# Kernel tuning notes

Hardware: AMD Instinct MI355X
Metric: run time of the kernel (lower is better)

Reference implementation:

```python
import jax, jax.numpy as jnp
import numpy as np

B, S, U = 64, 64, 16
EMB = 10
D = U - 2 + 2 * EMB      # encoder d_model = 34
DD = 3                   # decoder d_model
FF = 4                   # dim_feedforward
NL = 4                   # num layers (enc and dec)
ENH = 2                  # encoder heads
WV, SV = 10000, 400      # word / syllable vocab sizes


def _ln(x, w, b, eps=1e-5):
    mu = jnp.mean(x, -1, keepdims=True)
    var = jnp.mean((x - mu) ** 2, -1, keepdims=True)
    return (x - mu) / jnp.sqrt(var + eps) * w + b


def _mha(xq, xkv, qkv_w, qkv_b, out_w, out_b, nhead, mask=None):
    d = xq.shape[-1]
    wq, wk, wv = jnp.split(qkv_w, 3, axis=0)
    bq, bk, bv = jnp.split(qkv_b, 3, axis=0)
    q = xq @ wq.T + bq
    k = xkv @ wk.T + bk
    v = xkv @ wv.T + bv
    b_, sq, sk = q.shape[0], q.shape[1], k.shape[1]
    dh = d // nhead
    q = q.reshape(b_, sq, nhead, dh)
    k = k.reshape(b_, sk, nhead, dh)
    v = v.reshape(b_, sk, nhead, dh)
    scores = jnp.einsum('bqhd,bkhd->bhqk', q, k) * (1.0 / np.sqrt(dh))
    if mask is not None:
        scores = scores + mask
    attn = jax.nn.softmax(scores, axis=-1)
    out = jnp.einsum('bhqk,bkhd->bqhd', attn, v).reshape(b_, sq, d)
    return out @ out_w.T + out_b


def _pos_encoding(batch, d_model):
    # Faithful to the original quirk: pe has shape [max_len, 1, d] and is added
    # to a batch-first [B,S,D] tensor as x + pe[:B]  ->  row b of pe is added
    # to ALL sequence positions of batch element b.
    pos = jnp.arange(batch, dtype=jnp.float32)[:, None]
    div = jnp.exp(jnp.arange(0, d_model, 2, dtype=jnp.float32) * (-np.log(10000.0) / d_model))
    ang = pos * div  # [B, D/2]
    pe = jnp.stack([jnp.sin(ang), jnp.cos(ang)], axis=-1).reshape(batch, d_model)
    return pe[:, None, :]  # [B,1,D]


def setup_inputs() -> dict:
    key = jax.random.key(0)
    ks = iter(jax.random.split(key, 64))

    def n(shape, s=0.1):
        return jax.random.normal(next(ks), shape, dtype=jnp.float32) * s

    base = jax.random.uniform(next(ks), (B, S, U), dtype=jnp.float32)
    widx = jax.random.randint(next(ks), (B, S), 0, WV).astype(jnp.float32)
    sidx = jax.random.randint(next(ks), (B, S), 0, SV).astype(jnp.float32)
    src = base.at[:, :, U - 2].set(widx).at[:, :, U - 1].set(sidx)
    return {
        'src': src,
        'word_emb': jax.random.uniform(next(ks), (WV, EMB), jnp.float32, -0.1, 0.1),
        'syll_emb': jax.random.uniform(next(ks), (SV, EMB), jnp.float32, -0.1, 0.1),
        'enc_qkv_w': n((NL, 3 * D, D)), 'enc_qkv_b': jnp.zeros((NL, 3 * D)),
        'enc_out_w': n((NL, D, D)), 'enc_out_b': jnp.zeros((NL, D)),
        'enc_ln1_w': jnp.ones((NL, D)), 'enc_ln1_b': jnp.zeros((NL, D)),
        'enc_lin1_w': n((NL, FF, D)), 'enc_lin1_b': jnp.zeros((NL, FF)),
        'enc_lin2_w': n((NL, D, FF)), 'enc_lin2_b': jnp.zeros((NL, D)),
        'enc_ln2_w': jnp.ones((NL, D)), 'enc_ln2_b': jnp.zeros((NL, D)),
        'norm_w': jnp.ones((D,)), 'norm_b': jnp.zeros((D,)),
        'eo_w': jax.random.uniform(next(ks), (DD, D), jnp.float32, -0.1, 0.1),
        'eo_b': jnp.zeros((DD,)),
        'dec_sa_qkv_w': n((NL, 3 * DD, DD)), 'dec_sa_qkv_b': jnp.zeros((NL, 3 * DD)),
        'dec_sa_out_w': n((NL, DD, DD)), 'dec_sa_out_b': jnp.zeros((NL, DD)),
        'dec_ln1_w': jnp.ones((NL, DD)), 'dec_ln1_b': jnp.zeros((NL, DD)),
        'dec_ca_qkv_w': n((NL, 3 * DD, DD)), 'dec_ca_qkv_b': jnp.zeros((NL, 3 * DD)),
        'dec_ca_out_w': n((NL, DD, DD)), 'dec_ca_out_b': jnp.zeros((NL, DD)),
        'dec_ln2_w': jnp.ones((NL, DD)), 'dec_ln2_b': jnp.zeros((NL, DD)),
        'dec_lin1_w': n((NL, FF, DD)), 'dec_lin1_b': jnp.zeros((NL, FF)),
        'dec_lin2_w': n((NL, DD, FF)), 'dec_lin2_b': jnp.zeros((NL, DD)),
        'dec_ln3_w': jnp.ones((NL, DD)), 'dec_ln3_b': jnp.zeros((NL, DD)),
    }


def reference(src, word_emb, syll_emb,
              enc_qkv_w, enc_qkv_b, enc_out_w, enc_out_b,
              enc_ln1_w, enc_ln1_b, enc_lin1_w, enc_lin1_b,
              enc_lin2_w, enc_lin2_b, enc_ln2_w, enc_ln2_b,
              norm_w, norm_b, eo_w, eo_b,
              dec_sa_qkv_w, dec_sa_qkv_b, dec_sa_out_w, dec_sa_out_b,
              dec_ln1_w, dec_ln1_b,
              dec_ca_qkv_w, dec_ca_qkv_b, dec_ca_out_w, dec_ca_out_b,
              dec_ln2_w, dec_ln2_b,
              dec_lin1_w, dec_lin1_b, dec_lin2_w, dec_lin2_b,
              dec_ln3_w, dec_ln3_b):
    b, s = src.shape[0], src.shape[1]
    # embed_lyrics
    widx = src[:, :, U - 2].astype(jnp.int32)
    sidx = src[:, :, U - 1].astype(jnp.int32)
    x = jnp.concatenate([src[:, :, :U - 2], word_emb[widx], syll_emb[sidx]], axis=2)  # [B,S,D]
    x = x + _pos_encoding(b, D)
    # TransformerEncoder (post-norm, relu, dropout=0) + final LayerNorm
    for l in range(NL):
        sa = _mha(x, x, enc_qkv_w[l], enc_qkv_b[l], enc_out_w[l], enc_out_b[l], ENH)
        x = _ln(x + sa, enc_ln1_w[l], enc_ln1_b[l])
        ff = jax.nn.relu(x @ enc_lin1_w[l].T + enc_lin1_b[l]) @ enc_lin2_w[l].T + enc_lin2_b[l]
        x = _ln(x + ff, enc_ln2_w[l], enc_ln2_b[l])
    x = _ln(x, norm_w, norm_b)
    memory = x @ eo_w.T + eo_b  # [B,S,3]

    causal = jnp.where(jnp.tril(jnp.ones((s, s), bool)), 0.0, -1e9).astype(jnp.float32)

    def decode(tgt):
        y = tgt
        for l in range(NL):
            sa = _mha(y, y, dec_sa_qkv_w[l], dec_sa_qkv_b[l], dec_sa_out_w[l], dec_sa_out_b[l], 1, causal)
            y = _ln(y + sa, dec_ln1_w[l], dec_ln1_b[l])
            ca = _mha(y, memory, dec_ca_qkv_w[l], dec_ca_qkv_b[l], dec_ca_out_w[l], dec_ca_out_b[l], 1)
            y = _ln(y + ca, dec_ln2_w[l], dec_ln2_b[l])
            ff = jax.nn.relu(y @ dec_lin1_w[l].T + dec_lin1_b[l]) @ dec_lin2_w[l].T + dec_lin2_b[l]
            y = _ln(y + ff, dec_ln3_w[l], dec_ln3_b[l])
        return y

    # mask, position i only depends on tgt[:, :i+1], so a fixed-size padded
    # buffer + scan computes identical values.
    def step(tgt, i):
        out_i = jax.lax.dynamic_slice_in_dim(decode(tgt), i, 1, axis=1)  # [B,1,3]
        return jax.lax.dynamic_update_slice(tgt, out_i, (0, i + 1, 0)), None

    tgt0 = jnp.zeros((b, s, DD), jnp.float32)
    tgt, _ = jax.lax.scan(step, tgt0, jnp.arange(s - 1))
    return jnp.concatenate([tgt, src[:, :, U - 2:U - 1], src[:, :, U - 1:U]], axis=2)
```

## Files before the change

### kernel.cpp

```cpp
#include <hip/hip_runtime.h>
#include <math.h>

#define B_ 64
#define S_ 64
#define U_ 16
#define EMB_ 10
#define D_ 34
#define DD_ 3
#define FF_ 4
#define NL_ 4

__global__ __launch_bounds__(512) void enc_kernel(
    const float* __restrict__ src, const float* __restrict__ wemb,
    const float* __restrict__ semb,
    const float* __restrict__ qkv_w, const float* __restrict__ qkv_b,
    const float* __restrict__ out_w, const float* __restrict__ out_b,
    const float* __restrict__ ln1_w, const float* __restrict__ ln1_b,
    const float* __restrict__ lin1_w, const float* __restrict__ lin1_b,
    const float* __restrict__ lin2_w, const float* __restrict__ lin2_b,
    const float* __restrict__ ln2_w, const float* __restrict__ ln2_b,
    const float* __restrict__ norm_w, const float* __restrict__ norm_b,
    const float* __restrict__ eo_w, const float* __restrict__ eo_b,
    float* __restrict__ mem, float* __restrict__ out)
{
    const int b = blockIdx.x;
    const int tid = threadIdx.x;
    const int wv_ = tid >> 6;
    const int lane = tid & 63;

    __shared__ float xs[S_][D_ + 1];
    __shared__ float tmp[S_][D_ + 1];
    __shared__ float att[S_][D_ + 1];
    __shared__ __align__(16) float qsh[2][S_][21];
    __shared__ __align__(16) float ksh[2][S_][20];
    __shared__ __align__(16) float vsh[2][S_][20];
    __shared__ float ffh[S_][5];
    __shared__ float pacc[4][128][19];
    __shared__ float wq_s[3 * D_ * D_];
    __shared__ float wo_s[D_ * D_];
    __shared__ float w1_s[FF_ * D_];
    __shared__ float w2_s[D_ * FF_];
    __shared__ float bq_s[3 * D_], bo_s[D_], b1_s[FF_], b2_s[D_];
    __shared__ float l1w_s[D_], l1b_s[D_], l2w_s[D_], l2b_s[D_];

    const float negln = -logf(10000.0f) / (float)D_;
    #pragma unroll
    for (int rep = 0; rep < 5; ++rep) {
        int idx = tid + rep * 512;
        if (idx < S_ * D_) {
            int pos = idx / D_, d = idx % D_;
            float v;
            if (d < U_ - 2) {
                v = src[(b * S_ + pos) * U_ + d];
            } else if (d < U_ - 2 + EMB_) {
                int wi = (int)src[(b * S_ + pos) * U_ + (U_ - 2)];
                v = wemb[wi * EMB_ + (d - (U_ - 2))];
            } else {
                int si = (int)src[(b * S_ + pos) * U_ + (U_ - 1)];
                v = semb[si * EMB_ + (d - (U_ - 2 + EMB_))];
            }
            int k = d >> 1;
            float div = expf((float)(2 * k) * negln);
            float ang = (float)b * div;
            v += (d & 1) ? cosf(ang) : sinf(ang);
            xs[pos][d] = v;
        }
    }
    __syncthreads();

    const float rs17 = 0.24253562503633297f;

    for (int l = 0; l < NL_; ++l) {
        for (int t = tid; t < 3 * D_ * D_; t += 512) wq_s[t] = qkv_w[l * 3 * D_ * D_ + t];
        for (int t = tid; t < D_ * D_; t += 512)     wo_s[t] = out_w[l * D_ * D_ + t];
        for (int t = tid; t < FF_ * D_; t += 512)    w1_s[t] = lin1_w[l * FF_ * D_ + t];
        for (int t = tid; t < D_ * FF_; t += 512)    w2_s[t] = lin2_w[l * D_ * FF_ + t];
        for (int t = tid; t < 3 * D_ + 6 * D_ + FF_; t += 512) {
            if      (t < 3 * D_)          bq_s[t]            = qkv_b[l * 3 * D_ + t];
            else if (t < 3 * D_ + D_)     bo_s[t - 3 * D_]   = out_b[l * D_ + (t - 3 * D_)];
            else if (t < 3 * D_ + 2 * D_) l1w_s[t - 4 * D_]  = ln1_w[l * D_ + (t - 4 * D_)];
            else if (t < 3 * D_ + 3 * D_) l1b_s[t - 5 * D_]  = ln1_b[l * D_ + (t - 5 * D_)];
            else if (t < 3 * D_ + 4 * D_) l2w_s[t - 6 * D_]  = ln2_w[l * D_ + (t - 6 * D_)];
            else if (t < 3 * D_ + 5 * D_) l2b_s[t - 7 * D_]  = ln2_b[l * D_ + (t - 7 * D_)];
            else if (t < 3 * D_ + 6 * D_) b2_s[t - 8 * D_]   = lin2_b[l * D_ + (t - 8 * D_)];
            else                          b1_s[t - 9 * D_]   = lin1_b[l * FF_ + (t - 9 * D_)];
        }
        __syncthreads();

        for (int r = wv_; r < 3 * D_; r += 8) {
            const float* wrow = wq_s + r * D_;
            float aE = bq_s[r], aO = 0.f;
            #pragma unroll
            for (int d = 0; d < D_; d += 2) {
                aE += xs[lane][d] * wrow[d];
                aO += xs[lane][d + 1] * wrow[d + 1];
            }
            float acc = aE + aO;
            if (r < D_) {
                int h = (r >= 17), dd = r - h * 17;
                qsh[h][lane][dd] = acc;
            } else if (r < 2 * D_) {
                int rr = r - D_; int h = (rr >= 17), dd = rr - h * 17;
                ksh[h][lane][dd] = acc;
            } else {
                int rr = r - 2 * D_; int h = (rr >= 17), dd = rr - h * 17;
                vsh[h][lane][dd] = acc;
            }
        }
        __syncthreads();

        {
            int c = tid >> 7, hq = tid & 127;
            int h = hq >> 6, qi = hq & 63;
            float qv[17], acc[17];
            #pragma unroll
            for (int d = 0; d < 17; ++d) { qv[d] = qsh[h][qi][d]; acc[d] = 0.f; }
            float ssum = 0.f;
            int j0 = c * 16;
            for (int jj = 0; jj < 16; ++jj) {
                int j = j0 + jj;
                const float4* kr = (const float4*)ksh[h][j];
                const float4* vr = (const float4*)vsh[h][j];
                float4 k0 = kr[0], k1 = kr[1], k2 = kr[2], k3 = kr[3];
                float  k16 = ksh[h][j][16];
                float4 v0 = vr[0], v1 = vr[1], v2 = vr[2], v3 = vr[3];
                float  v16 = vsh[h][j][16];
                float sE = qv[0]*k0.x + qv[2]*k0.z + qv[4]*k1.x + qv[6]*k1.z +
                           qv[8]*k2.x + qv[10]*k2.z + qv[12]*k3.x + qv[14]*k3.z;
                float sO = qv[1]*k0.y + qv[3]*k0.w + qv[5]*k1.y + qv[7]*k1.w +
                           qv[9]*k2.y + qv[11]*k2.w + qv[13]*k3.y + qv[15]*k3.w;
                float sc = sE + sO + qv[16]*k16;
                float e = __expf(sc * rs17);
                ssum += e;
                acc[0] += e*v0.x;  acc[1] += e*v0.y;  acc[2] += e*v0.z;  acc[3] += e*v0.w;
                acc[4] += e*v1.x;  acc[5] += e*v1.y;  acc[6] += e*v1.z;  acc[7] += e*v1.w;
                acc[8] += e*v2.x;  acc[9] += e*v2.y;  acc[10] += e*v2.z; acc[11] += e*v2.w;
                acc[12] += e*v3.x; acc[13] += e*v3.y; acc[14] += e*v3.z; acc[15] += e*v3.w;
                acc[16] += e*v16;
            }
            #pragma unroll
            for (int d = 0; d < 17; ++d) pacc[c][hq][d] = acc[d];
            pacc[c][hq][17] = ssum;
        }
        __syncthreads();

        if (tid < 128) {
            int h = tid >> 6, qi = tid & 63;
            int off = h * 17;
            float ssum = pacc[0][tid][17] + pacc[1][tid][17] +
                         pacc[2][tid][17] + pacc[3][tid][17];
            float inv = 1.f / ssum;
            #pragma unroll
            for (int d = 0; d < 17; ++d)
                att[qi][off + d] = (pacc[0][tid][d] + pacc[1][tid][d] +
                                    pacc[2][tid][d] + pacc[3][tid][d]) * inv;
        }
        __syncthreads();

        for (int d = wv_; d < D_; d += 8) {
            const float* wrow = wo_s + d * D_;
            float aE = bo_s[d], aO = 0.f;
            #pragma unroll
            for (int e = 0; e < D_; e += 2) {
                aE += att[lane][e] * wrow[e];
                aO += att[lane][e + 1] * wrow[e + 1];
            }
            tmp[lane][d] = xs[lane][d] + aE + aO;
        }
        __syncthreads();

        if (tid < S_) {
            int row = tid;
            float sA = 0.f, sB = 0.f;
            #pragma unroll
            for (int d = 0; d < D_; d += 2) { sA += tmp[row][d]; sB += tmp[row][d + 1]; }
            float mu = (sA + sB) * (1.0f / D_);
            float vA = 0.f, vB = 0.f;
            #pragma unroll
            for (int d = 0; d < D_; d += 2) {
                float t0 = tmp[row][d] - mu;     vA += t0 * t0;
                float t1 = tmp[row][d + 1] - mu; vB += t1 * t1;
            }
            float rstd = rsqrtf((vA + vB) * (1.0f / D_) + 1e-5f);
            #pragma unroll
            for (int d = 0; d < D_; ++d)
                xs[row][d] = (tmp[row][d] - mu) * rstd * l1w_s[d] + l1b_s[d];
        }
        __syncthreads();

        if (tid < 256) {
            int pos = tid >> 2, f = tid & 3;
            const float* wrow = w1_s + f * D_;
            float aE = b1_s[f], aO = 0.f;
            #pragma unroll
            for (int d = 0; d < D_; d += 2) {
                aE += xs[pos][d] * wrow[d];
                aO += xs[pos][d + 1] * wrow[d + 1];
            }
            ffh[pos][f] = fmaxf(aE + aO, 0.f);
        }
        __syncthreads();

        for (int d = wv_; d < D_; d += 8) {
            const float* wrow = w2_s + d * FF_;
            float acc = b2_s[d] + ffh[lane][0] * wrow[0] + ffh[lane][1] * wrow[1] +
                        ffh[lane][2] * wrow[2] + ffh[lane][3] * wrow[3];
            tmp[lane][d] = xs[lane][d] + acc;
        }
        __syncthreads();

        if (tid < S_) {
            int row = tid;
            float sA = 0.f, sB = 0.f;
            #pragma unroll
            for (int d = 0; d < D_; d += 2) { sA += tmp[row][d]; sB += tmp[row][d + 1]; }
            float mu = (sA + sB) * (1.0f / D_);
            float vA = 0.f, vB = 0.f;
            #pragma unroll
            for (int d = 0; d < D_; d += 2) {
                float t0 = tmp[row][d] - mu;     vA += t0 * t0;
                float t1 = tmp[row][d + 1] - mu; vB += t1 * t1;
            }
            float rstd = rsqrtf((vA + vB) * (1.0f / D_) + 1e-5f);
            #pragma unroll
            for (int d = 0; d < D_; ++d)
                xs[row][d] = (tmp[row][d] - mu) * rstd * l2w_s[d] + l2b_s[d];
        }
        __syncthreads();
    }

    if (tid < S_) {
        int row = tid;
        float sA = 0.f, sB = 0.f;
        #pragma unroll
        for (int d = 0; d < D_; d += 2) { sA += xs[row][d]; sB += xs[row][d + 1]; }
        float mu = (sA + sB) * (1.0f / D_);
        float vA = 0.f, vB = 0.f;
        #pragma unroll
        for (int d = 0; d < D_; d += 2) {
            float t0 = xs[row][d] - mu;     vA += t0 * t0;
            float t1 = xs[row][d + 1] - mu; vB += t1 * t1;
        }
        float rstd = rsqrtf((vA + vB) * (1.0f / D_) + 1e-5f);
        #pragma unroll
        for (int d = 0; d < D_; ++d)
            xs[row][d] = (xs[row][d] - mu) * rstd * norm_w[d] + norm_b[d];
    }
    __syncthreads();

    if (tid < S_ * DD_) {
        int pos = tid / DD_, r = tid % DD_;
        const float* wrow = eo_w + r * D_;
        float aE = eo_b[r], aO = 0.f;
        #pragma unroll
        for (int d = 0; d < D_; d += 2) {
            aE += xs[pos][d] * wrow[d];
            aO += xs[pos][d + 1] * wrow[d + 1];
        }
        mem[(b * S_ + pos) * DD_ + r] = aE + aO;
    }

    if (tid < S_) {
        out[(b * S_ + tid) * 5 + 3] = src[(b * S_ + tid) * U_ + (U_ - 2)];
        out[(b * S_ + tid) * 5 + 4] = src[(b * S_ + tid) * U_ + (U_ - 1)];
    }
}

#define PIN(x) asm volatile("" : "+v"(x))

template <int CTRL>
__device__ __forceinline__ float dpp_add(float v) {
    int t = __builtin_amdgcn_update_dpp(0, __float_as_int(v), CTRL, 0xf, 0xf, true);
    return v + __int_as_float(t);
}

__device__ __forceinline__ float wave_sum_l63(float v) {
    v = dpp_add<0x111>(v);
    v = dpp_add<0x112>(v);
    v = dpp_add<0x114>(v);
    v = dpp_add<0x118>(v);
    v = dpp_add<0x142>(v);
    v = dpp_add<0x143>(v);
    return v;
}

__device__ __forceinline__ float bcast63(float v) {
    return __int_as_float(__builtin_amdgcn_readlane(__float_as_int(v), 63));
}

__device__ __forceinline__ void ln3e(float z0, float z1, float z2,
                                     float w0, float w1, float w2,
                                     float b0, float b1, float b2,
                                     float& o0, float& o1, float& o2) {
    float s1 = (z0 + z1) + z2;
    float s2 = fmaf(z0, z0, fmaf(z1, z1, z2 * z2));
    float mu = s1 * (1.0f / 3.0f);
    float vpe = fmaf(s2, (1.0f / 3.0f), fmaf(-mu, mu, 1e-5f));
    float rstd = __builtin_amdgcn_rsqf(vpe);
    o0 = fmaf(z0 - mu, rstd * w0, b0);
    o1 = fmaf(z1 - mu, rstd * w1, b1);
    o2 = fmaf(z2 - mu, rstd * w2, b2);
}

__global__ __launch_bounds__(64, 1) void dec_kernel(
    const float* __restrict__ mem,
    const float* __restrict__ sa_qkv_w, const float* __restrict__ sa_qkv_b,
    const float* __restrict__ sa_out_w, const float* __restrict__ sa_out_b,
    const float* __restrict__ gln1_w, const float* __restrict__ gln1_b,
    const float* __restrict__ ca_qkv_w, const float* __restrict__ ca_qkv_b,
    const float* __restrict__ ca_out_w, const float* __restrict__ ca_out_b,
    const float* __restrict__ gln2_w, const float* __restrict__ gln2_b,
    const float* __restrict__ l1_w, const float* __restrict__ l1_b,
    const float* __restrict__ l2_w, const float* __restrict__ l2_b,
    const float* __restrict__ gln3_w, const float* __restrict__ gln3_b,
    float* __restrict__ out)
{
    const int b = blockIdx.x;
    const int lane = threadIdx.x;
    const float LOG2E = 1.4426950408889634f;
    const float rs3 = 0.5773502691896258f;
    const float QS = rs3 * LOG2E;

    __shared__ __align__(16) float fst[NL_][60];
    for (int t = lane; t < NL_ * 60; t += 64) {
        int l = t / 60, s = t % 60;
        float v = 0.f;
        if      (s < 9)  v = ca_qkv_w[l * 27 + s];
        else if (s < 12) v = ca_qkv_b[l * 9 + (s - 9)];
        else if (s < 15) v = ca_out_b[l * 3 + (s - 12)];
        else if (s < 18) v = gln2_w[l * 3 + (s - 15)];
        else if (s < 21) v = gln2_b[l * 3 + (s - 18)];
        else if (s < 33) v = l1_w[l * 12 + (s - 21)];
        else if (s < 37) v = l1_b[l * 4 + (s - 33)];
        else if (s < 49) v = l2_w[l * 12 + (s - 37)];
        else if (s < 52) v = l2_b[l * 3 + (s - 49)];
        else if (s < 55) v = gln3_w[l * 3 + (s - 52)];
        else if (s < 58) v = gln3_b[l * 3 + (s - 55)];
        fst[l][s] = v;
    }
    __syncthreads();

    float Wqp[NL_][3][3], Bqp[NL_][3];
    float Wk [NL_][3][3], Bk [NL_][3];
    float WVp[NL_][3][3], bvp[NL_][3];
    float Bso[NL_][3];
    float N1w[NL_][3], N1b[NL_][3];

    #pragma unroll
    for (int l = 0; l < NL_; ++l) {
        #pragma unroll
        for (int r = 0; r < 3; ++r) {
            Bqp[l][r] = sa_qkv_b[l * 9 + r] * QS;
            Bk [l][r] = sa_qkv_b[l * 9 + 3 + r];
            #pragma unroll
            for (int c = 0; c < 3; ++c) {
                Wqp[l][r][c] = sa_qkv_w[l * 27 + r * 3 + c] * QS;
                Wk [l][r][c] = sa_qkv_w[l * 27 + (3 + r) * 3 + c];
            }
            float a0 = 0.f, a1 = 0.f, a2 = 0.f, ab = 0.f;
            #pragma unroll
            for (int t = 0; t < 3; ++t) {
                float wso = sa_out_w[l * 9 + r * 3 + t];
                a0 += wso * sa_qkv_w[l * 27 + (6 + t) * 3 + 0];
                a1 += wso * sa_qkv_w[l * 27 + (6 + t) * 3 + 1];
                a2 += wso * sa_qkv_w[l * 27 + (6 + t) * 3 + 2];
                ab += wso * sa_qkv_b[l * 9 + 6 + t];
            }
            WVp[l][r][0] = a0; WVp[l][r][1] = a1; WVp[l][r][2] = a2;
            bvp[l][r] = ab;
            Bso[l][r] = sa_out_b[l * 3 + r];
            N1w[l][r] = gln1_w[l * 3 + r];  N1b[l][r] = gln1_b[l * 3 + r];
        }
    }

    float m0 = mem[(b * S_ + lane) * DD_ + 0];
    float m1 = mem[(b * S_ + lane) * DD_ + 1];
    float m2 = mem[(b * S_ + lane) * DD_ + 2];

    float ck[NL_][3], cvp[NL_][3];
    #pragma unroll
    for (int l = 0; l < NL_; ++l) {
        float cvt[3];
        #pragma unroll
        for (int t = 0; t < 3; ++t) {
            cvt[t] = ca_qkv_w[l * 27 + (6 + t) * 3 + 0] * m0 +
                     ca_qkv_w[l * 27 + (6 + t) * 3 + 1] * m1 +
                     ca_qkv_w[l * 27 + (6 + t) * 3 + 2] * m2 + ca_qkv_b[l * 9 + 6 + t];
        }
        #pragma unroll
        for (int r = 0; r < 3; ++r) {
            float kk = ca_qkv_w[l * 27 + (3 + r) * 3 + 0] * m0 +
                       ca_qkv_w[l * 27 + (3 + r) * 3 + 1] * m1 +
                       ca_qkv_w[l * 27 + (3 + r) * 3 + 2] * m2 + ca_qkv_b[l * 9 + 3 + r];
            ck[l][r] = kk * QS;
            cvp[l][r] = ca_out_w[l * 9 + r * 3 + 0] * cvt[0] +
                        ca_out_w[l * 9 + r * 3 + 1] * cvt[1] +
                        ca_out_w[l * 9 + r * 3 + 2] * cvt[2];
        }
    }

    #pragma unroll
    for (int l = 0; l < NL_; ++l) {
        #pragma unroll
        for (int r = 0; r < 3; ++r) {
            PIN(Bqp[l][r]); PIN(Bk[l][r]); PIN(bvp[l][r]); PIN(Bso[l][r]);
            PIN(N1w[l][r]); PIN(N1b[l][r]);
            PIN(ck[l][r]); PIN(cvp[l][r]);
            #pragma unroll
            for (int c = 0; c < 3; ++c) {
                PIN(Wqp[l][r][c]); PIN(Wk[l][r][c]); PIN(WVp[l][r][c]);
            }
        }
    }

    float sk[NL_][3] = {{0.f}}, sv[NL_][3] = {{0.f}};

    if (lane < 3) out[(b * S_ + 0) * 5 + lane] = 0.f;

    float y0 = 0.f, y1 = 0.f, y2 = 0.f;

    for (int i = 0; i < S_ - 1; ++i) {
        float msa = (lane <= i) ? 0.f : -1.0e30f;
        #pragma unroll
        for (int l = 0; l < NL_; ++l) {
            float wv[60];
            {
                const float4* fp = (const float4*)fst[l];
                #pragma unroll
                for (int k = 0; k < 15; ++k) {
                    float4 t4 = fp[k];
                    wv[4 * k + 0] = t4.x; wv[4 * k + 1] = t4.y;
                    wv[4 * k + 2] = t4.z; wv[4 * k + 3] = t4.w;
                }
            }

            float q0 = fmaf(Wqp[l][0][0], y0, fmaf(Wqp[l][0][1], y1, fmaf(Wqp[l][0][2], y2, Bqp[l][0])));
            float q1 = fmaf(Wqp[l][1][0], y0, fmaf(Wqp[l][1][1], y1, fmaf(Wqp[l][1][2], y2, Bqp[l][1])));
            float q2 = fmaf(Wqp[l][2][0], y0, fmaf(Wqp[l][2][1], y1, fmaf(Wqp[l][2][2], y2, Bqp[l][2])));
            float k0 = fmaf(Wk[l][0][0], y0, fmaf(Wk[l][0][1], y1, fmaf(Wk[l][0][2], y2, Bk[l][0])));
            float k1 = fmaf(Wk[l][1][0], y0, fmaf(Wk[l][1][1], y1, fmaf(Wk[l][1][2], y2, Bk[l][1])));
            float k2 = fmaf(Wk[l][2][0], y0, fmaf(Wk[l][2][1], y1, fmaf(Wk[l][2][2], y2, Bk[l][2])));
            float v0 = fmaf(WVp[l][0][0], y0, fmaf(WVp[l][0][1], y1, fmaf(WVp[l][0][2], y2, bvp[l][0])));
            float v1 = fmaf(WVp[l][1][0], y0, fmaf(WVp[l][1][1], y1, fmaf(WVp[l][1][2], y2, bvp[l][1])));
            float v2 = fmaf(WVp[l][2][0], y0, fmaf(WVp[l][2][1], y1, fmaf(WVp[l][2][2], y2, bvp[l][2])));
            if (lane == i) {
                sk[l][0] = k0; sk[l][1] = k1; sk[l][2] = k2;
                sv[l][0] = v0; sv[l][1] = v1; sv[l][2] = v2;
            }
            float sc = fmaf(q0, sk[l][0], fmaf(q1, sk[l][1], fmaf(q2, sk[l][2], msa)));
            float e = __builtin_amdgcn_exp2f(sc);
            float es  = bcast63(wave_sum_l63(e));
            float ev0 = bcast63(wave_sum_l63(e * sv[l][0]));
            float ev1 = bcast63(wave_sum_l63(e * sv[l][1]));
            float ev2 = bcast63(wave_sum_l63(e * sv[l][2]));
            float t0 = y0 + Bso[l][0], t1 = y1 + Bso[l][1], t2 = y2 + Bso[l][2];
            float z0 = fmaf(t0, es, ev0);
            float z1 = fmaf(t1, es, ev1);
            float z2 = fmaf(t2, es, ev2);
            ln3e(z0, z1, z2, N1w[l][0], N1w[l][1], N1w[l][2],
                 N1b[l][0], N1b[l][1], N1b[l][2], y0, y1, y2);

            float p0 = fmaf(wv[0], y0, fmaf(wv[1], y1, fmaf(wv[2], y2, wv[9])));
            float p1 = fmaf(wv[3], y0, fmaf(wv[4], y1, fmaf(wv[5], y2, wv[10])));
            float p2 = fmaf(wv[6], y0, fmaf(wv[7], y1, fmaf(wv[8], y2, wv[11])));
            float sc2 = fmaf(p0, ck[l][0], fmaf(p1, ck[l][1], p2 * ck[l][2]));
            float e2 = __builtin_amdgcn_exp2f(sc2);
            float cs  = bcast63(wave_sum_l63(e2));
            float cw0 = bcast63(wave_sum_l63(e2 * cvp[l][0]));
            float cw1 = bcast63(wave_sum_l63(e2 * cvp[l][1]));
            float cw2 = bcast63(wave_sum_l63(e2 * cvp[l][2]));
            float u0 = y0 + wv[12], u1 = y1 + wv[13], u2 = y2 + wv[14];
            z0 = fmaf(u0, cs, cw0);
            z1 = fmaf(u1, cs, cw1);
            z2 = fmaf(u2, cs, cw2);
            ln3e(z0, z1, z2, wv[15], wv[16], wv[17],
                 wv[18], wv[19], wv[20], y0, y1, y2);

            float h0 = fmaxf(fmaf(wv[21], y0, fmaf(wv[22], y1, fmaf(wv[23], y2, wv[33]))), 0.f);
            float h1 = fmaxf(fmaf(wv[24], y0, fmaf(wv[25], y1, fmaf(wv[26], y2, wv[34]))), 0.f);
            float h2 = fmaxf(fmaf(wv[27], y0, fmaf(wv[28], y1, fmaf(wv[29], y2, wv[35]))), 0.f);
            float h3 = fmaxf(fmaf(wv[30], y0, fmaf(wv[31], y1, fmaf(wv[32], y2, wv[36]))), 0.f);
            float f0 = fmaf(wv[37], h0, fmaf(wv[38], h1, fmaf(wv[39], h2, fmaf(wv[40], h3, wv[49]))));
            float f1 = fmaf(wv[41], h0, fmaf(wv[42], h1, fmaf(wv[43], h2, fmaf(wv[44], h3, wv[50]))));
            float f2 = fmaf(wv[45], h0, fmaf(wv[46], h1, fmaf(wv[47], h2, fmaf(wv[48], h3, wv[51]))));
            ln3e(y0 + f0, y1 + f1, y2 + f2, wv[52], wv[53], wv[54],
                 wv[55], wv[56], wv[57], y0, y1, y2);
        }
        if (lane == 0) {
            out[(b * S_ + i + 1) * 5 + 0] = y0;
            out[(b * S_ + i + 1) * 5 + 1] = y1;
            out[(b * S_ + i + 1) * 5 + 2] = y2;
        }
    }
}

extern "C" void kernel_launch(void* const* d_in, const int* in_sizes, int n_in,
                              void* d_out, int out_size, void* d_ws, size_t ws_size,
                              hipStream_t stream) {
    const float* src  = (const float*)d_in[0];
    const float* wemb = (const float*)d_in[1];
    const float* semb = (const float*)d_in[2];

    float* mem = (float*)d_ws;
    float* out = (float*)d_out;

    enc_kernel<<<B_, 512, 0, stream>>>(
        src, wemb, semb,
        (const float*)d_in[3],  (const float*)d_in[4],
        (const float*)d_in[5],  (const float*)d_in[6],
        (const float*)d_in[7],  (const float*)d_in[8],
        (const float*)d_in[9],  (const float*)d_in[10],
        (const float*)d_in[11], (const float*)d_in[12],
        (const float*)d_in[13], (const float*)d_in[14],
        (const float*)d_in[15], (const float*)d_in[16],
        (const float*)d_in[17], (const float*)d_in[18],
        mem, out);

    dec_kernel<<<B_, 64, 0, stream>>>(
        mem,
        (const float*)d_in[19], (const float*)d_in[20],
        (const float*)d_in[21], (const float*)d_in[22],
        (const float*)d_in[23], (const float*)d_in[24],
        (const float*)d_in[25], (const float*)d_in[26],
        (const float*)d_in[27], (const float*)d_in[28],
        (const float*)d_in[29], (const float*)d_in[30],
        (const float*)d_in[31], (const float*)d_in[32],
        (const float*)d_in[33], (const float*)d_in[34],
        (const float*)d_in[35], (const float*)d_in[36],
        out);
}
```

Before: 367.1 us.

## Read encoder weights via scalar loads and move decoder params to shared

The encoder no longer stages per-layer weights in LDS. Each wave reads its weight row straight from global memory using a wave-uniform readfirstlane index, so the loads become scalar, and the activation row is cached in registers. This removes the staging copy and one barrier per layer. The decoder moves the self-attention output bias and LN1 parameters out of pinned registers into the shared parameter table, split into two chunks to lower register pressure. Positional encoding also switches to fast-math intrinsics, which may slightly change precision.

```diff
diff --git a/kernel.cpp b/kernel.cpp
--- a/kernel.cpp
+++ b/kernel.cpp
@@ -36,12 +36,6 @@
     __shared__ __align__(16) float vsh[2][S_][20];
     __shared__ float ffh[S_][5];
     __shared__ float pacc[4][128][19];
-    __shared__ float wq_s[3 * D_ * D_];
-    __shared__ float wo_s[D_ * D_];
-    __shared__ float w1_s[FF_ * D_];
-    __shared__ float w2_s[D_ * FF_];
-    __shared__ float bq_s[3 * D_], bo_s[D_], b1_s[FF_], b2_s[D_];
-    __shared__ float l1w_s[D_], l1b_s[D_], l2w_s[D_], l2b_s[D_];
 
     const float negln = -logf(10000.0f) / (float)D_;
     #pragma unroll
@@ -60,9 +54,9 @@
                 v = semb[si * EMB_ + (d - (U_ - 2 + EMB_))];
             }
             int k = d >> 1;
-            float div = expf((float)(2 * k) * negln);
+            float div = __expf((float)(2 * k) * negln);
             float ang = (float)b * div;
-            v += (d & 1) ? cosf(ang) : sinf(ang);
+            v += (d & 1) ? __cosf(ang) : __sinf(ang);
             xs[pos][d] = v;
         }
     }
@@ -71,40 +65,29 @@
     const float rs17 = 0.24253562503633297f;
 
     for (int l = 0; l < NL_; ++l) {
-        for (int t = tid; t < 3 * D_ * D_; t += 512) wq_s[t] = qkv_w[l * 3 * D_ * D_ + t];
-        for (int t = tid; t < D_ * D_; t += 512)     wo_s[t] = out_w[l * D_ * D_ + t];
-        for (int t = tid; t < FF_ * D_; t += 512)    w1_s[t] = lin1_w[l * FF_ * D_ + t];
-        for (int t = tid; t < D_ * FF_; t += 512)    w2_s[t] = lin2_w[l * D_ * FF_ + t];
-        for (int t = tid; t < 3 * D_ + 6 * D_ + FF_; t += 512) {
-            if      (t < 3 * D_)          bq_s[t]            = qkv_b[l * 3 * D_ + t];
-            else if (t < 3 * D_ + D_)     bo_s[t - 3 * D_]   = out_b[l * D_ + (t - 3 * D_)];
-            else if (t < 3 * D_ + 2 * D_) l1w_s[t - 4 * D_]  = ln1_w[l * D_ + (t - 4 * D_)];
-            else if (t < 3 * D_ + 3 * D_) l1b_s[t - 5 * D_]  = ln1_b[l * D_ + (t - 5 * D_)];
-            else if (t < 3 * D_ + 4 * D_) l2w_s[t - 6 * D_]  = ln2_w[l * D_ + (t - 6 * D_)];
-            else if (t < 3 * D_ + 5 * D_) l2b_s[t - 7 * D_]  = ln2_b[l * D_ + (t - 7 * D_)];
-            else if (t < 3 * D_ + 6 * D_) b2_s[t - 8 * D_]   = lin2_b[l * D_ + (t - 8 * D_)];
-            else                          b1_s[t - 9 * D_]   = lin1_b[l * FF_ + (t - 9 * D_)];
-        }
-        __syncthreads();
-
-        for (int r = wv_; r < 3 * D_; r += 8) {
-            const float* wrow = wq_s + r * D_;
-            float aE = bq_s[r], aO = 0.f;
-            #pragma unroll
-            for (int d = 0; d < D_; d += 2) {
-                aE += xs[lane][d] * wrow[d];
-                aO += xs[lane][d + 1] * wrow[d + 1];
-            }
-            float acc = aE + aO;
-            if (r < D_) {
-                int h = (r >= 17), dd = r - h * 17;
-                qsh[h][lane][dd] = acc;
-            } else if (r < 2 * D_) {
-                int rr = r - D_; int h = (rr >= 17), dd = rr - h * 17;
-                ksh[h][lane][dd] = acc;
-            } else {
-                int rr = r - 2 * D_; int h = (rr >= 17), dd = rr - h * 17;
-                vsh[h][lane][dd] = acc;
+        const float* Wq = qkv_w + l * 3 * D_ * D_;
+        const float* Bq = qkv_b + l * 3 * D_;
+
+        {
+            float xr[D_];
+            #pragma unroll
+            for (int d = 0; d < D_; ++d) xr[d] = xs[lane][d];
+            for (int rb = 0; rb < 13; ++rb) {
+                int r = wv_ + (rb << 3);
+                if (r < 3 * D_) {
+                    int ru = __builtin_amdgcn_readfirstlane(r);
+                    const float* wrow = Wq + ru * D_;
+                    float aE = Bq[ru], aO = 0.f;
+                    #pragma unroll
+                    for (int d = 0; d < D_; d += 2) {
+                        aE = fmaf(xr[d], wrow[d], aE);
+                        aO = fmaf(xr[d + 1], wrow[d + 1], aO);
+                    }
+                    float acc = aE + aO;
+                    if (ru < D_)          { int h = (ru >= 17), dd = ru - h * 17; qsh[h][lane][dd] = acc; }
+                    else if (ru < 2 * D_) { int rr = ru - D_;     int h = (rr >= 17), dd = rr - h * 17; ksh[h][lane][dd] = acc; }
+                    else                  { int rr = ru - 2 * D_; int h = (rr >= 17), dd = rr - h * 17; vsh[h][lane][dd] = acc; }
+                }
             }
         }
         __syncthreads();
@@ -157,15 +140,26 @@
         }
         __syncthreads();
 
-        for (int d = wv_; d < D_; d += 8) {
-            const float* wrow = wo_s + d * D_;
-            float aE = bo_s[d], aO = 0.f;
-            #pragma unroll
-            for (int e = 0; e < D_; e += 2) {
-                aE += att[lane][e] * wrow[e];
-                aO += att[lane][e + 1] * wrow[e + 1];
-            }
-            tmp[lane][d] = xs[lane][d] + aE + aO;
+        {
+            float ar[D_];
+            #pragma unroll
+            for (int e = 0; e < D_; ++e) ar[e] = att[lane][e];
+            const float* Wo = out_w + l * D_ * D_;
+            const float* Bo = out_b + l * D_;
+            for (int rb = 0; rb < 5; ++rb) {
+                int d = wv_ + (rb << 3);
+                if (d < D_) {
+                    int du = __builtin_amdgcn_readfirstlane(d);
+                    const float* wrow = Wo + du * D_;
+                    float aE = Bo[du], aO = 0.f;
+                    #pragma unroll
+                    for (int e = 0; e < D_; e += 2) {
+                        aE = fmaf(ar[e], wrow[e], aE);
+                        aO = fmaf(ar[e + 1], wrow[e + 1], aO);
+                    }
+                    tmp[lane][du] = xs[lane][du] + aE + aO;
+                }
+            }
         }
         __syncthreads();
 
@@ -184,28 +178,38 @@
             float rstd = rsqrtf((vA + vB) * (1.0f / D_) + 1e-5f);
             #pragma unroll
             for (int d = 0; d < D_; ++d)
-                xs[row][d] = (tmp[row][d] - mu) * rstd * l1w_s[d] + l1b_s[d];
-        }
-        __syncthreads();
-
-        if (tid < 256) {
-            int pos = tid >> 2, f = tid & 3;
-            const float* wrow = w1_s + f * D_;
-            float aE = b1_s[f], aO = 0.f;
+                xs[row][d] = (tmp[row][d] - mu) * rstd * ln1_w[l * D_ + d] + ln1_b[l * D_ + d];
+        }
+        __syncthreads();
+
+        if (wv_ < 4) {
+            int fu = __builtin_amdgcn_readfirstlane(wv_);
+            const float* wrow = lin1_w + l * FF_ * D_ + fu * D_;
+            float aE = lin1_b[l * FF_ + fu], aO = 0.f;
             #pragma unroll
             for (int d = 0; d < D_; d += 2) {
-                aE += xs[pos][d] * wrow[d];
-                aO += xs[pos][d + 1] * wrow[d + 1];
-            }
-            ffh[pos][f] = fmaxf(aE + aO, 0.f);
-        }
-        __syncthreads();
-
-        for (int d = wv_; d < D_; d += 8) {
-            const float* wrow = w2_s + d * FF_;
-            float acc = b2_s[d] + ffh[lane][0] * wrow[0] + ffh[lane][1] * wrow[1] +
-                        ffh[lane][2] * wrow[2] + ffh[lane][3] * wrow[3];
-            tmp[lane][d] = xs[lane][d] + acc;
+                aE = fmaf(xs[lane][d], wrow[d], aE);
+                aO = fmaf(xs[lane][d + 1], wrow[d + 1], aO);
+            }
+            ffh[lane][fu] = fmaxf(aE + aO, 0.f);
+        }
+        __syncthreads();
+
+        {
+            float h0 = ffh[lane][0], h1 = ffh[lane][1],
+                  h2 = ffh[lane][2], h3 = ffh[lane][3];
+            const float* W2 = lin2_w + l * D_ * FF_;
+            const float* B2 = lin2_b + l * D_;
+            for (int rb = 0; rb < 5; ++rb) {
+                int d = wv_ + (rb << 3);
+                if (d < D_) {
+                    int du = __builtin_amdgcn_readfirstlane(d);
+                    const float* wrow = W2 + du * FF_;
+                    float acc = fmaf(h0, wrow[0], fmaf(h1, wrow[1],
+                                fmaf(h2, wrow[2], fmaf(h3, wrow[3], B2[du]))));
+                    tmp[lane][du] = xs[lane][du] + acc;
+                }
+            }
         }
         __syncthreads();
 
@@ -224,7 +228,7 @@
             float rstd = rsqrtf((vA + vB) * (1.0f / D_) + 1e-5f);
             #pragma unroll
             for (int d = 0; d < D_; ++d)
-                xs[row][d] = (tmp[row][d] - mu) * rstd * l2w_s[d] + l2b_s[d];
+                xs[row][d] = (tmp[row][d] - mu) * rstd * ln2_w[l * D_ + d] + ln2_b[l * D_ + d];
         }
         __syncthreads();
     }
@@ -248,16 +252,16 @@
     }
     __syncthreads();
 
-    if (tid < S_ * DD_) {
-        int pos = tid / DD_, r = tid % DD_;
-        const float* wrow = eo_w + r * D_;
-        float aE = eo_b[r], aO = 0.f;
+    if (wv_ < 3) {
+        int ru = __builtin_amdgcn_readfirstlane(wv_);
+        const float* wrow = eo_w + ru * D_;
+        float aE = eo_b[ru], aO = 0.f;
         #pragma unroll
         for (int d = 0; d < D_; d += 2) {
-            aE += xs[pos][d] * wrow[d];
-            aO += xs[pos][d + 1] * wrow[d + 1];
-        }
-        mem[(b * S_ + pos) * DD_ + r] = aE + aO;
+            aE = fmaf(xs[lane][d], wrow[d], aE);
+            aO = fmaf(xs[lane][d + 1], wrow[d + 1], aO);
+        }
+        mem[(b * S_ + lane) * DD_ + ru] = aE + aO;
     }
 
     if (tid < S_) {
@@ -321,21 +325,25 @@
     const float rs3 = 0.5773502691896258f;
     const float QS = rs3 * LOG2E;
 
-    __shared__ __align__(16) float fst[NL_][60];
-    for (int t = lane; t < NL_ * 60; t += 64) {
-        int l = t / 60, s = t % 60;
+    __shared__ __align__(16) float fst[NL_][72];
+    for (int t = lane; t < NL_ * 72; t += 64) {
+        int l = t / 72, s = t % 72;
         float v = 0.f;
-        if      (s < 9)  v = ca_qkv_w[l * 27 + s];
-        else if (s < 12) v = ca_qkv_b[l * 9 + (s - 9)];
-        else if (s < 15) v = ca_out_b[l * 3 + (s - 12)];
-        else if (s < 18) v = gln2_w[l * 3 + (s - 15)];
-        else if (s < 21) v = gln2_b[l * 3 + (s - 18)];
-        else if (s < 33) v = l1_w[l * 12 + (s - 21)];
-        else if (s < 37) v = l1_b[l * 4 + (s - 33)];
-        else if (s < 49) v = l2_w[l * 12 + (s - 37)];
-        else if (s < 52) v = l2_b[l * 3 + (s - 49)];
-        else if (s < 55) v = gln3_w[l * 3 + (s - 52)];
-        else if (s < 58) v = gln3_b[l * 3 + (s - 55)];
+        if      (s < 3)  v = sa_out_b[l * 3 + s];
+        else if (s < 6)  v = gln1_w[l * 3 + (s - 3)];
+        else if (s < 9)  v = gln1_b[l * 3 + (s - 6)];
+        else if (s < 18) v = ca_qkv_w[l * 27 + (s - 9)];
+        else if (s < 21) v = ca_qkv_b[l * 9 + (s - 18)];
+        else if (s < 24) v = ca_out_b[l * 3 + (s - 21)];
+        else if (s < 27) v = gln2_w[l * 3 + (s - 24)];
+        else if (s < 30) v = gln2_b[l * 3 + (s - 27)];
+        else if (s < 32) v = 0.f;
+        else if (s < 44) v = l1_w[l * 12 + (s - 32)];
+        else if (s < 48) v = l1_b[l * 4 + (s - 44)];
+        else if (s < 60) v = l2_w[l * 12 + (s - 48)];
+        else if (s < 63) v = l2_b[l * 3 + (s - 60)];
+        else if (s < 66) v = gln3_w[l * 3 + (s - 63)];
+        else if (s < 69) v = gln3_b[l * 3 + (s - 66)];
         fst[l][s] = v;
     }
     __syncthreads();
@@ -343,8 +351,6 @@
     float Wqp[NL_][3][3], Bqp[NL_][3];
     float Wk [NL_][3][3], Bk [NL_][3];
     float WVp[NL_][3][3], bvp[NL_][3];
-    float Bso[NL_][3];
-    float N1w[NL_][3], N1b[NL_][3];
 
     #pragma unroll
     for (int l = 0; l < NL_; ++l) {
@@ -368,8 +374,6 @@
             }
             WVp[l][r][0] = a0; WVp[l][r][1] = a1; WVp[l][r][2] = a2;
             bvp[l][r] = ab;
-            Bso[l][r] = sa_out_b[l * 3 + r];
-            N1w[l][r] = gln1_w[l * 3 + r];  N1b[l][r] = gln1_b[l * 3 + r];
         }
     }
 
@@ -403,8 +407,7 @@
     for (int l = 0; l < NL_; ++l) {
         #pragma unroll
         for (int r = 0; r < 3; ++r) {
-            PIN(Bqp[l][r]); PIN(Bk[l][r]); PIN(bvp[l][r]); PIN(Bso[l][r]);
-            PIN(N1w[l][r]); PIN(N1b[l][r]);
+            PIN(Bqp[l][r]); PIN(Bk[l][r]); PIN(bvp[l][r]);
             PIN(ck[l][r]); PIN(cvp[l][r]);
             #pragma unroll
             for (int c = 0; c < 3; ++c) {
@@ -423,14 +426,14 @@
         float msa = (lane <= i) ? 0.f : -1.0e30f;
         #pragma unroll
         for (int l = 0; l < NL_; ++l) {
-            float wv[60];
+            float wa[32];
             {
                 const float4* fp = (const float4*)fst[l];
                 #pragma unroll
-                for (int k = 0; k < 15; ++k) {
+                for (int k = 0; k < 8; ++k) {
                     float4 t4 = fp[k];
-                    wv[4 * k + 0] = t4.x; wv[4 * k + 1] = t4.y;
-                    wv[4 * k + 2] = t4.z; wv[4 * k + 3] = t4.w;
+                    wa[4 * k + 0] = t4.x; wa[4 * k + 1] = t4.y;
+                    wa[4 * k + 2] = t4.z; wa[4 * k + 3] = t4.w;
                 }
             }
 
@@ -449,42 +452,54 @@
             }
             float sc = fmaf(q0, sk[l][0], fmaf(q1, sk[l][1], fmaf(q2, sk[l][2], msa)));
             float e = __builtin_amdgcn_exp2f(sc);
+
+            float wb[40];
+            {
+                const float4* fp = (const float4*)&fst[l][32];
+                #pragma unroll
+                for (int k = 0; k < 10; ++k) {
+                    float4 t4 = fp[k];
+                    wb[4 * k + 0] = t4.x; wb[4 * k + 1] = t4.y;
+                    wb[4 * k + 2] = t4.z; wb[4 * k + 3] = t4.w;
+                }
+            }
+
             float es  = bcast63(wave_sum_l63(e));
             float ev0 = bcast63(wave_sum_l63(e * sv[l][0]));
             float ev1 = bcast63(wave_sum_l63(e * sv[l][1]));
             float ev2 = bcast63(wave_sum_l63(e * sv[l][2]));
-            float t0 = y0 + Bso[l][0], t1 = y1 + Bso[l][1], t2 = y2 + Bso[l][2];
+            float t0 = y0 + wa[0], t1 = y1 + wa[1], t2 = y2 + wa[2];
             float z0 = fmaf(t0, es, ev0);
             float z1 = fmaf(t1, es, ev1);
             float z2 = fmaf(t2, es, ev2);
-            ln3e(z0, z1, z2, N1w[l][0], N1w[l][1], N1w[l][2],
-                 N1b[l][0], N1b[l][1], N1b[l][2], y0, y1, y2);
-
-            float p0 = fmaf(wv[0], y0, fmaf(wv[1], y1, fmaf(wv[2], y2, wv[9])));
-            float p1 = fmaf(wv[3], y0, fmaf(wv[4], y1, fmaf(wv[5], y2, wv[10])));
-            float p2 = fmaf(wv[6], y0, fmaf(wv[7], y1, fmaf(wv[8], y2, wv[11])));
+            ln3e(z0, z1, z2, wa[3], wa[4], wa[5], wa[6], wa[7], wa[8],
+                 y0, y1, y2);
+
+            float p0 = fmaf(wa[9],  y0, fmaf(wa[10], y1, fmaf(wa[11], y2, wa[18])));
+            float p1 = fmaf(wa[12], y0, fmaf(wa[13], y1, fmaf(wa[14], y2, wa[19])));
+            float p2 = fmaf(wa[15], y0, fmaf(wa[16], y1, fmaf(wa[17], y2, wa[20])));
             float sc2 = fmaf(p0, ck[l][0], fmaf(p1, ck[l][1], p2 * ck[l][2]));
             float e2 = __builtin_amdgcn_exp2f(sc2);
             float cs  = bcast63(wave_sum_l63(e2));
             float cw0 = bcast63(wave_sum_l63(e2 * cvp[l][0]));
             float cw1 = bcast63(wave_sum_l63(e2 * cvp[l][1]));
             float cw2 = bcast63(wave_sum_l63(e2 * cvp[l][2]));
-            float u0 = y0 + wv[12], u1 = y1 + wv[13], u2 = y2 + wv[14];
+            float u0 = y0 + wa[21], u1 = y1 + wa[22], u2 = y2 + wa[23];
             z0 = fmaf(u0, cs, cw0);
             z1 = fmaf(u1, cs, cw1);
             z2 = fmaf(u2, cs, cw2);
-            ln3e(z0, z1, z2, wv[15], wv[16], wv[17],
-                 wv[18], wv[19], wv[20], y0, y1, y2);
-
-            float h0 = fmaxf(fmaf(wv[21], y0, fmaf(wv[22], y1, fmaf(wv[23], y2, wv[33]))), 0.f);
-            float h1 = fmaxf(fmaf(wv[24], y0, fmaf(wv[25], y1, fmaf(wv[26], y2, wv[34]))), 0.f);
-            float h2 = fmaxf(fmaf(wv[27], y0, fmaf(wv[28], y1, fmaf(wv[29], y2, wv[35]))), 0.f);
-            float h3 = fmaxf(fmaf(wv[30], y0, fmaf(wv[31], y1, fmaf(wv[32], y2, wv[36]))), 0.f);
-            float f0 = fmaf(wv[37], h0, fmaf(wv[38], h1, fmaf(wv[39], h2, fmaf(wv[40], h3, wv[49]))));
-            float f1 = fmaf(wv[41], h0, fmaf(wv[42], h1, fmaf(wv[43], h2, fmaf(wv[44], h3, wv[50]))));
-            float f2 = fmaf(wv[45], h0, fmaf(wv[46], h1, fmaf(wv[47], h2, fmaf(wv[48], h3, wv[51]))));
-            ln3e(y0 + f0, y1 + f1, y2 + f2, wv[52], wv[53], wv[54],
-                 wv[55], wv[56], wv[57], y0, y1, y2);
+            ln3e(z0, z1, z2, wa[24], wa[25], wa[26], wa[27], wa[28], wa[29],
+                 y0, y1, y2);
+
+            float h0 = fmaxf(fmaf(wb[0], y0, fmaf(wb[1],  y1, fmaf(wb[2],  y2, wb[12]))), 0.f);
+            float h1 = fmaxf(fmaf(wb[3], y0, fmaf(wb[4],  y1, fmaf(wb[5],  y2, wb[13]))), 0.f);
+            float h2 = fmaxf(fmaf(wb[6], y0, fmaf(wb[7],  y1, fmaf(wb[8],  y2, wb[14]))), 0.f);
+            float h3 = fmaxf(fmaf(wb[9], y0, fmaf(wb[10], y1, fmaf(wb[11], y2, wb[15]))), 0.f);
+            float f0 = fmaf(wb[16], h0, fmaf(wb[17], h1, fmaf(wb[18], h2, fmaf(wb[19], h3, wb[28]))));
+            float f1 = fmaf(wb[20], h0, fmaf(wb[21], h1, fmaf(wb[22], h2, fmaf(wb[23], h3, wb[29]))));
+            float f2 = fmaf(wb[24], h0, fmaf(wb[25], h1, fmaf(wb[26], h2, fmaf(wb[27], h3, wb[30]))));
+            ln3e(y0 + f0, y1 + f1, y2 + f2, wb[31], wb[32], wb[33],
+                 wb[34], wb[35], wb[36], y0, y1, y2);
         }
         if (lane == 0) {
             out[(b * S_ + i + 1) * 5 + 0] = y0;
```

Measured after the change: 366.5 us. About the same (-0.2%).
